# Optimization experiments

Measured on AMD Instinct MI355X. Metric: run time of the kernel, lower is better.

## Reference

```python
import jax, jax.numpy as jnp
import numpy as np

EMBED_DIM = 1024
N_HEADS = 16
HEAD_DIM = EMBED_DIM // N_HEADS


def setup_inputs() -> dict:
    key = jax.random.key(0)
    ks = jax.random.split(key, 5)
    B, T, C = 4, 2048, EMBED_DIM
    s = 0.02
    return {
        "x": jax.random.normal(ks[0], (B, T, C), dtype=jnp.float32),
        "w_qkv": jax.random.normal(ks[1], (C, 3 * C), dtype=jnp.float32) * s,
        "b_qkv": jnp.zeros((3 * C,), dtype=jnp.float32),
        "w_proj": jax.random.normal(ks[2], (C, C), dtype=jnp.float32) * s,
        "b_proj": jnp.zeros((C,), dtype=jnp.float32),
    }


def reference(x, w_qkv, b_qkv, w_proj, b_proj):
    B, T, C = x.shape
    H, D = N_HEADS, HEAD_DIM
    qkv = x @ w_qkv + b_qkv  # [B,T,3C]
    q, k, v = jnp.split(qkv, 3, axis=-1)
    # [B,H,T,D]
    q = q.reshape(B, T, H, D).transpose(0, 2, 1, 3)
    k = k.reshape(B, T, H, D).transpose(0, 2, 1, 3)
    v = v.reshape(B, T, H, D).transpose(0, 2, 1, 3)
    scale = jnp.asarray(D, x.dtype) ** -0.5
    att = jnp.einsum("bhqd,bhkd->bhqk", q, k) * scale  # [B,H,T,T]
    causal = jnp.tril(jnp.ones((T, T), dtype=bool))
    att = jnp.where(causal, att, jnp.asarray(-jnp.inf, att.dtype))
    att = jax.nn.softmax(att, axis=-1)
    out = jnp.einsum("bhqk,bhkd->bhqd", att, v)  # [B,H,T,D]
    out = out.transpose(0, 2, 1, 3).reshape(B, T, C)
    return out @ w_proj + b_proj
```

## Files before the change

kernel.cpp:

```cpp
#include <hip/hip_runtime.h>
#include <hip/hip_bf16.h>


typedef __bf16 bf16x8 __attribute__((ext_vector_type(8)));
typedef float f32x4 __attribute__((ext_vector_type(4)));
typedef unsigned short u16x8 __attribute__((ext_vector_type(8)));
typedef unsigned short u16x4 __attribute__((ext_vector_type(4)));
typedef unsigned int u32;

#define LOG2E 1.44269504088896340736f
#define NEG_INF (-__builtin_inff())

#define AS_GLOBAL(p) ((const __attribute__((address_space(1))) u32*)(p))
#define AS_LDS(p) ((__attribute__((address_space(3))) u32*)(p))

__device__ __forceinline__ unsigned short f2bf(float f) {
  unsigned int u = __builtin_bit_cast(unsigned int, f);
  u += 0x7fff + ((u >> 16) & 1);
  return (unsigned short)(u >> 16);
}

__device__ __forceinline__ u32 cvt_pk_bf16(float lo, float hi) {
  u32 r;
  asm("v_cvt_pk_bf16_f32 %0, %1, %2" : "=v"(r) : "v"(lo), "v"(hi));
  return r;
}

__device__ __forceinline__ bf16x8 ld_frag(const unsigned short* p) {
  return __builtin_bit_cast(bf16x8, *reinterpret_cast<const u16x8*>(p));
}

__global__ void k_convert(const float* __restrict__ in, unsigned short* __restrict__ out, int n4) {
  int i = blockIdx.x * blockDim.x + threadIdx.x;
  int stride = gridDim.x * blockDim.x;
  for (; i < n4; i += stride) {
    float4 v = reinterpret_cast<const float4*>(in)[i];
    u16x4 o = { f2bf(v.x), f2bf(v.y), f2bf(v.z), f2bf(v.w) };
    reinterpret_cast<u16x4*>(out)[i] = o;
  }
}

__global__ void k_transpose(const float* __restrict__ in, unsigned short* __restrict__ out,
                            int K, int N, int scaleN, float scl) {
  __shared__ float tile[32][33];
  int n0 = blockIdx.x * 32, k0 = blockIdx.y * 32;
  int tx = threadIdx.x & 31, ty = threadIdx.x >> 5;
#pragma unroll
  for (int i = 0; i < 4; i++)
    tile[ty + i * 8][tx] = in[(size_t)(k0 + ty + i * 8) * N + n0 + tx];
  __syncthreads();
#pragma unroll
  for (int i = 0; i < 4; i++) {
    int n = n0 + ty + i * 8;
    float v = tile[tx][ty + i * 8];
    if (n < scaleN) v *= scl;
    out[(size_t)n * K + k0 + tx] = f2bf(v);
  }
}

__global__ void k_scale_bias(const float* __restrict__ in, float* __restrict__ out,
                             int n, int scaleN, float scl) {
  int i = blockIdx.x * blockDim.x + threadIdx.x;
  if (i < n) out[i] = (i < scaleN) ? in[i] * scl : in[i];
}

template <bool BF16_OUT>
__global__ __launch_bounds__(256) void k_gemm(
    const unsigned short* __restrict__ A, const unsigned short* __restrict__ Bt,
    const float* __restrict__ bias, void* __restrict__ Cv, int M, int N, int K) {
  constexpr int BK = 64;
  __shared__ unsigned short Asm[128][BK];
  __shared__ unsigned short Bsm[128][BK];
  const int tid = threadIdx.x;
  const int lane = tid & 63, w = tid >> 6;
  const int wr = w >> 1, wc = w & 1;
  const int brow = blockIdx.x * 128, bcol = blockIdx.y * 128;
  const int r0 = lane & 15, kq = lane >> 4;

  f32x4 acc[4][4] = {};

  const int srow = lane >> 3;
  const int scol = ((lane & 7) ^ srow) * 8;
  const int swa = (r0 & 7) << 3;

  for (int k0 = 0; k0 < K; k0 += BK) {
    __syncthreads();
#pragma unroll
    for (int q2 = 0; q2 < 4; q2++) {
      int c = w * 4 + q2;
      const unsigned short* ga = &A[(size_t)(brow + c * 8 + srow) * K + k0 + scol];
      const unsigned short* gb = &Bt[(size_t)(bcol + c * 8 + srow) * K + k0 + scol];
      __builtin_amdgcn_global_load_lds(AS_GLOBAL(ga), AS_LDS(&Asm[c * 8][0]), 16, 0, 0);
      __builtin_amdgcn_global_load_lds(AS_GLOBAL(gb), AS_LDS(&Bsm[c * 8][0]), 16, 0, 0);
    }
    __syncthreads();
#pragma unroll
    for (int c = 0; c < 2; c++) {
      bf16x8 af[4], bfr[4];
#pragma unroll
      for (int m = 0; m < 4; m++)
        af[m] = ld_frag(&Asm[wr * 64 + m * 16 + r0][(c * 32 + kq * 8) ^ swa]);
#pragma unroll
      for (int n = 0; n < 4; n++)
        bfr[n] = ld_frag(&Bsm[wc * 64 + n * 16 + r0][(c * 32 + kq * 8) ^ swa]);
      __builtin_amdgcn_s_setprio(1);
#pragma unroll
      for (int m = 0; m < 4; m++)
#pragma unroll
        for (int n = 0; n < 4; n++)
          acc[m][n] = __builtin_amdgcn_mfma_f32_16x16x32_bf16(af[m], bfr[n], acc[m][n], 0, 0, 0);
      __builtin_amdgcn_s_setprio(0);
    }
  }

  const int orow = kq * 4;
#pragma unroll
  for (int n = 0; n < 4; n++) {
#pragma unroll
    for (int m = 0; m < 4; m++) {
      int col = bcol + wc * 64 + n * 16 + r0;
      float bv = bias[col];
#pragma unroll
      for (int r = 0; r < 4; r++) {
        int row = brow + wr * 64 + m * 16 + orow + r;
        float v = acc[m][n][r] + bv;
        if (BF16_OUT)
          ((unsigned short*)Cv)[(size_t)row * N + col] = f2bf(v);
        else
          ((float*)Cv)[(size_t)row * N + col] = v;
      }
    }
  }
}

__global__ __launch_bounds__(256, 3) void k_flash(const unsigned short* __restrict__ qkv,
                                                  unsigned short* __restrict__ att, int T) {
  constexpr int C3 = 3072, C = 1024;
  __shared__ unsigned short Ksm[2][64][72];
  __shared__ unsigned short Vsm[2][64][72];

  const int tid = threadIdx.x, lane = tid & 63, w = tid >> 6;
  const int bh = blockIdx.x;
  const int qtp = gridDim.y - 1 - blockIdx.y;
  const int b = bh >> 4, h = bh & 15;
  const int q0 = qtp * 128;
  const int r0 = lane & 15, kq = lane >> 4;

  const size_t rowbase = (size_t)b * T * C3;
  const int qb0 = q0 + w * 32, qb1 = qb0 + 16;

  bf16x8 qf[2][2];
  {
    const unsigned short* qp0 = &qkv[rowbase + (size_t)(qb0 + r0) * C3 + h * 64];
    qf[0][0] = ld_frag(&qp0[kq * 8]);
    qf[0][1] = ld_frag(&qp0[32 + kq * 8]);
    const unsigned short* qp1 = qp0 + (size_t)16 * C3;
    qf[1][0] = ld_frag(&qp1[kq * 8]);
    qf[1][1] = ld_frag(&qp1[32 + kq * 8]);
  }

  f32x4 accO[2][4] = {};
  f32x4 ls4[2] = {{0.f,0.f,0.f,0.f},{0.f,0.f,0.f,0.f}};
  float m_run[2] = {NEG_INF, NEG_INF};

  const int stk = tid >> 3, sd8 = (tid & 7) * 8;
  const unsigned short* kbase = &qkv[rowbase + (size_t)stk * C3 + h * 64 + sd8 + C];
  constexpr size_t PSTRIDE = (size_t)32 * C3;

  u16x8 kreg[2], vreg[2];
  auto LOADT = [&](size_t off) {
#pragma unroll
    for (int p = 0; p < 2; p++) {
      kreg[p] = *reinterpret_cast<const u16x8*>(kbase + off + p * PSTRIDE);
      vreg[p] = *reinterpret_cast<const u16x8*>(kbase + off + p * PSTRIDE + C);
    }
  };
  auto WRITET = [&](int buf) {
#pragma unroll
    for (int p = 0; p < 2; p++) {
      int tkk = p * 32 + stk;
      *reinterpret_cast<u16x8*>(&Ksm[buf][tkk][sd8]) = kreg[p];
      int tkx = tkk ^ sd8;
#pragma unroll
      for (int i = 0; i < 8; i++) Vsm[buf][sd8 + i][tkx] = vreg[p][i];
    }
  };

  auto TILE = [&](int buf, int k0) {
    if (k0 > qb1 + 15) return;
    const unsigned short(*Ks)[72] = Ksm[buf];
    const unsigned short(*Vs)[72] = Vsm[buf];

    f32x4 st[2][4];
    __builtin_amdgcn_s_setprio(1);
#pragma unroll
    for (int s = 0; s < 4; s++) {
      bf16x8 kf0 = ld_frag(&Ks[s * 16 + r0][kq * 8]);
      bf16x8 kf1 = ld_frag(&Ks[s * 16 + r0][32 + kq * 8]);
#pragma unroll
      for (int u = 0; u < 2; u++) {
        f32x4 a = {};
        a = __builtin_amdgcn_mfma_f32_16x16x32_bf16(kf0, qf[u][0], a, 0, 0, 0);
        a = __builtin_amdgcn_mfma_f32_16x16x32_bf16(kf1, qf[u][1], a, 0, 0, 0);
        st[u][s] = a;
      }
    }
    __builtin_amdgcn_s_setprio(0);

    u32 pd[2][2][4];
#pragma unroll
    for (int u = 0; u < 2; u++) {
      const int qbu = u ? qb1 : qb0;
      const int qmy = qbu + r0;
      f32x4 sv[4];
      if (k0 + 63 > qbu) {
#pragma unroll
        for (int s = 0; s < 4; s++)
#pragma unroll
          for (int r = 0; r < 4; r++) {
            int kg = k0 + s * 16 + kq * 4 + r;
            sv[s][r] = (kg > qmy) ? NEG_INF : st[u][s][r];
          }
      } else {
#pragma unroll
        for (int s = 0; s < 4; s++) sv[s] = st[u][s];
      }

      f32x4 m4 = __builtin_elementwise_max(__builtin_elementwise_max(sv[0], sv[1]),
                                           __builtin_elementwise_max(sv[2], sv[3]));
      float mx = fmaxf(fmaxf(m4[0], m4[1]), fmaxf(m4[2], m4[3]));

      if (__any(mx > m_run[u] + 8.f)) {
        mx = fmaxf(mx, __shfl_xor(mx, 16));
        mx = fmaxf(mx, __shfl_xor(mx, 32));
        float mn = fmaxf(m_run[u], mx);
        float corr = exp2f(m_run[u] - mn);
        m_run[u] = mn;
        ls4[u] *= corr;
        float cq[4];
#pragma unroll
        for (int r = 0; r < 4; r++) cq[r] = __shfl(corr, kq * 4 + r);
#pragma unroll
        for (int n = 0; n < 4; n++)
#pragma unroll
          for (int r = 0; r < 4; r++) accO[u][n][r] *= cq[r];
      }

#pragma unroll
      for (int s = 0; s < 4; s++) {
        f32x4 d = sv[s] - m_run[u];
        f32x4 p = { exp2f(d[0]), exp2f(d[1]), exp2f(d[2]), exp2f(d[3]) };
        sv[s] = p;
        ls4[u] += p;
      }
      pd[u][0][0] = cvt_pk_bf16(sv[0][0], sv[0][1]);
      pd[u][0][1] = cvt_pk_bf16(sv[0][2], sv[0][3]);
      pd[u][0][2] = cvt_pk_bf16(sv[1][0], sv[1][1]);
      pd[u][0][3] = cvt_pk_bf16(sv[1][2], sv[1][3]);
      pd[u][1][0] = cvt_pk_bf16(sv[2][0], sv[2][1]);
      pd[u][1][1] = cvt_pk_bf16(sv[2][2], sv[2][3]);
      pd[u][1][2] = cvt_pk_bf16(sv[3][0], sv[3][1]);
      pd[u][1][3] = cvt_pk_bf16(sv[3][2], sv[3][3]);
    }

    __builtin_amdgcn_s_setprio(1);
#pragma unroll
    for (int t = 0; t < 2; t++) {
      bf16x8 pa0 = __builtin_bit_cast(bf16x8, *reinterpret_cast<u16x8*>(pd[0][t]));
      bf16x8 pa1 = __builtin_bit_cast(bf16x8, *reinterpret_cast<u16x8*>(pd[1][t]));
#pragma unroll
      for (int n = 0; n < 4; n++) {
        int d = n * 16 + r0;
        int swzb = d & 56;
        const u16x4 lo = *reinterpret_cast<const u16x4*>(&Vs[d][(t * 32 + kq * 4) ^ swzb]);
        const u16x4 hi = *reinterpret_cast<const u16x4*>(&Vs[d][(t * 32 + 16 + kq * 4) ^ swzb]);
        u16x8 vbw;
#pragma unroll
        for (int i = 0; i < 4; i++) { vbw[i] = lo[i]; vbw[4 + i] = hi[i]; }
        bf16x8 vb = __builtin_bit_cast(bf16x8, vbw);
        accO[0][n] = __builtin_amdgcn_mfma_f32_16x16x32_bf16(pa0, vb, accO[0][n], 0, 0, 0);
        accO[1][n] = __builtin_amdgcn_mfma_f32_16x16x32_bf16(pa1, vb, accO[1][n], 0, 0, 0);
      }
    }
    __builtin_amdgcn_s_setprio(0);
  };

  int buf = 0;
  LOADT(0);
  WRITET(0);
  size_t koff = (size_t)64 * C3;
  const int nkt = (q0 + 128) >> 6;
  for (int kt = 0; kt < nkt - 1; kt++) {
    __syncthreads();
    LOADT(koff);
    koff += (size_t)64 * C3;
    TILE(buf, kt * 64);
    WRITET(buf ^ 1);
    buf ^= 1;
  }
  __syncthreads();
  TILE(buf, (nkt - 1) * 64);

#pragma unroll
  for (int u = 0; u < 2; u++) {
    const int qbu = u ? qb1 : qb0;
    float l = ls4[u][0] + ls4[u][1] + ls4[u][2] + ls4[u][3];
    l += __shfl_xor(l, 16);
    l += __shfl_xor(l, 32);
    float lr[4];
#pragma unroll
    for (int r = 0; r < 4; r++) lr[r] = 1.f / __shfl(l, kq * 4 + r);
#pragma unroll
    for (int n = 0; n < 4; n++) {
#pragma unroll
      for (int r = 0; r < 4; r++) {
        int qrow = qbu + kq * 4 + r;
        float v = accO[u][n][r] * lr[r];
        att[((size_t)b * T + qrow) * C + h * 64 + n * 16 + r0] = f2bf(v);
      }
    }
  }
}

extern "C" void kernel_launch(void* const* d_in, const int* in_sizes, int n_in,
                              void* d_out, int out_size, void* d_ws, size_t ws_size,
                              hipStream_t stream) {
  const float* x = (const float*)d_in[0];
  const float* w_qkv = (const float*)d_in[1];
  const float* b_qkv = (const float*)d_in[2];
  const float* w_proj = (const float*)d_in[3];
  const float* b_proj = (const float*)d_in[4];

  constexpr int B = 4, T = 2048, C = 1024, C3 = 3072;
  constexpr int M = B * T;
  constexpr float SCL = 0.125f * LOG2E;

  unsigned short* x_bf = (unsigned short*)d_ws;
  unsigned short* wqkvT = x_bf + (size_t)M * C;
  unsigned short* wprojT = wqkvT + (size_t)C3 * C;
  unsigned short* qkv = wprojT + (size_t)C * C;
  unsigned short* att = qkv + (size_t)M * C3;
  float* bias_s = (float*)(att + (size_t)M * C);

  hipLaunchKernelGGL(k_convert, dim3(2048), dim3(256), 0, stream, x, x_bf, M * C / 4);
  hipLaunchKernelGGL(k_transpose, dim3(C3 / 32, C / 32), dim3(256), 0, stream,
                     w_qkv, wqkvT, C, C3, C, SCL);
  hipLaunchKernelGGL(k_transpose, dim3(C / 32, C / 32), dim3(256), 0, stream,
                     w_proj, wprojT, C, C, 0, 1.f);
  hipLaunchKernelGGL(k_scale_bias, dim3((C3 + 255) / 256), dim3(256), 0, stream,
                     b_qkv, bias_s, C3, C, SCL);
  hipLaunchKernelGGL((k_gemm<true>), dim3(M / 128, C3 / 128), dim3(256), 0, stream,
                     x_bf, wqkvT, bias_s, (void*)qkv, M, C3, C);
  hipLaunchKernelGGL(k_flash, dim3(64, 16), dim3(256), 0, stream, qkv, att, T);
  hipLaunchKernelGGL((k_gemm<false>), dim3(M / 128, C / 128), dim3(256), 0, stream,
                     att, wprojT, b_proj, d_out, M, C, C);
}
```

Before: 166.9 us.

## Double flash-attention query tile to 256 rows per block for K/V reuse

Each flash-attention block now covers 256 query rows instead of 128, so each wave handles 64 rows across four 16-row sub-tiles. K/V tiles staged in LDS are reused across twice as many queries, which halves global K/V traffic and the number of blocks. Causal skipping is applied per pair of sub-tiles. The cost is higher register pressure, with launch bounds lowered to 2 blocks per CU, and only 512 blocks in the grid, which risks worse load balance across the causal triangle.

```diff
diff --git a/kernel.cpp b/kernel.cpp
--- a/kernel.cpp
+++ b/kernel.cpp
@@ -133,7 +133,7 @@
   }
 }
 
-__global__ __launch_bounds__(256, 3) void k_flash(const unsigned short* __restrict__ qkv,
+__global__ __launch_bounds__(256, 2) void k_flash(const unsigned short* __restrict__ qkv,
                                                   unsigned short* __restrict__ att, int T) {
   constexpr int C3 = 3072, C = 1024;
   __shared__ unsigned short Ksm[2][64][72];
@@ -143,25 +143,23 @@
   const int bh = blockIdx.x;
   const int qtp = gridDim.y - 1 - blockIdx.y;
   const int b = bh >> 4, h = bh & 15;
-  const int q0 = qtp * 128;
+  const int q0 = qtp * 256;
   const int r0 = lane & 15, kq = lane >> 4;
 
   const size_t rowbase = (size_t)b * T * C3;
-  const int qb0 = q0 + w * 32, qb1 = qb0 + 16;
-
-  bf16x8 qf[2][2];
-  {
-    const unsigned short* qp0 = &qkv[rowbase + (size_t)(qb0 + r0) * C3 + h * 64];
-    qf[0][0] = ld_frag(&qp0[kq * 8]);
-    qf[0][1] = ld_frag(&qp0[32 + kq * 8]);
-    const unsigned short* qp1 = qp0 + (size_t)16 * C3;
-    qf[1][0] = ld_frag(&qp1[kq * 8]);
-    qf[1][1] = ld_frag(&qp1[32 + kq * 8]);
-  }
-
-  f32x4 accO[2][4] = {};
-  f32x4 ls4[2] = {{0.f,0.f,0.f,0.f},{0.f,0.f,0.f,0.f}};
-  float m_run[2] = {NEG_INF, NEG_INF};
+  const int qb0 = q0 + w * 64;
+
+  bf16x8 qf[4][2];
+#pragma unroll
+  for (int u = 0; u < 4; u++) {
+    const unsigned short* qp = &qkv[rowbase + (size_t)(qb0 + u * 16 + r0) * C3 + h * 64];
+    qf[u][0] = ld_frag(&qp[kq * 8]);
+    qf[u][1] = ld_frag(&qp[32 + kq * 8]);
+  }
+
+  f32x4 accO[4][4] = {};
+  f32x4 ls4[4] = {{0.f,0.f,0.f,0.f},{0.f,0.f,0.f,0.f},{0.f,0.f,0.f,0.f},{0.f,0.f,0.f,0.f}};
+  float m_run[4] = {NEG_INF, NEG_INF, NEG_INF, NEG_INF};
 
   const int stk = tid >> 3, sd8 = (tid & 7) * 8;
   const unsigned short* kbase = &qkv[rowbase + (size_t)stk * C3 + h * 64 + sd8 + C];
@@ -187,87 +185,95 @@
   };
 
   auto TILE = [&](int buf, int k0) {
-    if (k0 > qb1 + 15) return;
+    if (k0 > qb0 + 63) return;
+    const bool p0 = (k0 <= qb0 + 31);
     const unsigned short(*Ks)[72] = Ksm[buf];
     const unsigned short(*Vs)[72] = Vsm[buf];
 
-    f32x4 st[2][4];
+    u32 pd[4][2][4];
+
+#pragma unroll
+    for (int pp = 0; pp < 2; pp++) {
+      if (pp == 0 && !p0) continue;
+      f32x4 st[2][4];
+      __builtin_amdgcn_s_setprio(1);
+#pragma unroll
+      for (int s = 0; s < 4; s++) {
+        bf16x8 kf0 = ld_frag(&Ks[s * 16 + r0][kq * 8]);
+        bf16x8 kf1 = ld_frag(&Ks[s * 16 + r0][32 + kq * 8]);
+#pragma unroll
+        for (int ui = 0; ui < 2; ui++) {
+          const int u = pp * 2 + ui;
+          f32x4 a = {};
+          a = __builtin_amdgcn_mfma_f32_16x16x32_bf16(kf0, qf[u][0], a, 0, 0, 0);
+          a = __builtin_amdgcn_mfma_f32_16x16x32_bf16(kf1, qf[u][1], a, 0, 0, 0);
+          st[ui][s] = a;
+        }
+      }
+      __builtin_amdgcn_s_setprio(0);
+
+#pragma unroll
+      for (int ui = 0; ui < 2; ui++) {
+        const int u = pp * 2 + ui;
+        const int qbu = qb0 + u * 16;
+        const int qmy = qbu + r0;
+        f32x4 sv[4];
+        if (k0 + 63 > qbu) {
+#pragma unroll
+          for (int s = 0; s < 4; s++)
+#pragma unroll
+            for (int r = 0; r < 4; r++) {
+              int kg = k0 + s * 16 + kq * 4 + r;
+              sv[s][r] = (kg > qmy) ? NEG_INF : st[ui][s][r];
+            }
+        } else {
+#pragma unroll
+          for (int s = 0; s < 4; s++) sv[s] = st[ui][s];
+        }
+
+        f32x4 m4 = __builtin_elementwise_max(__builtin_elementwise_max(sv[0], sv[1]),
+                                             __builtin_elementwise_max(sv[2], sv[3]));
+        float mx = fmaxf(fmaxf(m4[0], m4[1]), fmaxf(m4[2], m4[3]));
+
+        if (__any(mx > m_run[u] + 8.f)) {
+          mx = fmaxf(mx, __shfl_xor(mx, 16));
+          mx = fmaxf(mx, __shfl_xor(mx, 32));
+          float mn = fmaxf(m_run[u], mx);
+          float corr = exp2f(m_run[u] - mn);
+          m_run[u] = mn;
+          ls4[u] *= corr;
+          float cq[4];
+#pragma unroll
+          for (int r = 0; r < 4; r++) cq[r] = __shfl(corr, kq * 4 + r);
+#pragma unroll
+          for (int n = 0; n < 4; n++)
+#pragma unroll
+            for (int r = 0; r < 4; r++) accO[u][n][r] *= cq[r];
+        }
+
+#pragma unroll
+        for (int s = 0; s < 4; s++) {
+          f32x4 d = sv[s] - m_run[u];
+          f32x4 p = { exp2f(d[0]), exp2f(d[1]), exp2f(d[2]), exp2f(d[3]) };
+          sv[s] = p;
+          ls4[u] += p;
+        }
+        pd[u][0][0] = cvt_pk_bf16(sv[0][0], sv[0][1]);
+        pd[u][0][1] = cvt_pk_bf16(sv[0][2], sv[0][3]);
+        pd[u][0][2] = cvt_pk_bf16(sv[1][0], sv[1][1]);
+        pd[u][0][3] = cvt_pk_bf16(sv[1][2], sv[1][3]);
+        pd[u][1][0] = cvt_pk_bf16(sv[2][0], sv[2][1]);
+        pd[u][1][1] = cvt_pk_bf16(sv[2][2], sv[2][3]);
+        pd[u][1][2] = cvt_pk_bf16(sv[3][0], sv[3][1]);
+        pd[u][1][3] = cvt_pk_bf16(sv[3][2], sv[3][3]);
+      }
+    }
+
     __builtin_amdgcn_s_setprio(1);
 #pragma unroll
-    for (int s = 0; s < 4; s++) {
-      bf16x8 kf0 = ld_frag(&Ks[s * 16 + r0][kq * 8]);
-      bf16x8 kf1 = ld_frag(&Ks[s * 16 + r0][32 + kq * 8]);
-#pragma unroll
-      for (int u = 0; u < 2; u++) {
-        f32x4 a = {};
-        a = __builtin_amdgcn_mfma_f32_16x16x32_bf16(kf0, qf[u][0], a, 0, 0, 0);
-        a = __builtin_amdgcn_mfma_f32_16x16x32_bf16(kf1, qf[u][1], a, 0, 0, 0);
-        st[u][s] = a;
-      }
-    }
-    __builtin_amdgcn_s_setprio(0);
-
-    u32 pd[2][2][4];
-#pragma unroll
-    for (int u = 0; u < 2; u++) {
-      const int qbu = u ? qb1 : qb0;
-      const int qmy = qbu + r0;
-      f32x4 sv[4];
-      if (k0 + 63 > qbu) {
-#pragma unroll
-        for (int s = 0; s < 4; s++)
-#pragma unroll
-          for (int r = 0; r < 4; r++) {
-            int kg = k0 + s * 16 + kq * 4 + r;
-            sv[s][r] = (kg > qmy) ? NEG_INF : st[u][s][r];
-          }
-      } else {
-#pragma unroll
-        for (int s = 0; s < 4; s++) sv[s] = st[u][s];
-      }
-
-      f32x4 m4 = __builtin_elementwise_max(__builtin_elementwise_max(sv[0], sv[1]),
-                                           __builtin_elementwise_max(sv[2], sv[3]));
-      float mx = fmaxf(fmaxf(m4[0], m4[1]), fmaxf(m4[2], m4[3]));
-
-      if (__any(mx > m_run[u] + 8.f)) {
-        mx = fmaxf(mx, __shfl_xor(mx, 16));
-        mx = fmaxf(mx, __shfl_xor(mx, 32));
-        float mn = fmaxf(m_run[u], mx);
-        float corr = exp2f(m_run[u] - mn);
-        m_run[u] = mn;
-        ls4[u] *= corr;
-        float cq[4];
-#pragma unroll
-        for (int r = 0; r < 4; r++) cq[r] = __shfl(corr, kq * 4 + r);
-#pragma unroll
-        for (int n = 0; n < 4; n++)
-#pragma unroll
-          for (int r = 0; r < 4; r++) accO[u][n][r] *= cq[r];
-      }
-
-#pragma unroll
-      for (int s = 0; s < 4; s++) {
-        f32x4 d = sv[s] - m_run[u];
-        f32x4 p = { exp2f(d[0]), exp2f(d[1]), exp2f(d[2]), exp2f(d[3]) };
-        sv[s] = p;
-        ls4[u] += p;
-      }
-      pd[u][0][0] = cvt_pk_bf16(sv[0][0], sv[0][1]);
-      pd[u][0][1] = cvt_pk_bf16(sv[0][2], sv[0][3]);
-      pd[u][0][2] = cvt_pk_bf16(sv[1][0], sv[1][1]);
-      pd[u][0][3] = cvt_pk_bf16(sv[1][2], sv[1][3]);
-      pd[u][1][0] = cvt_pk_bf16(sv[2][0], sv[2][1]);
-      pd[u][1][1] = cvt_pk_bf16(sv[2][2], sv[2][3]);
-      pd[u][1][2] = cvt_pk_bf16(sv[3][0], sv[3][1]);
-      pd[u][1][3] = cvt_pk_bf16(sv[3][2], sv[3][3]);
-    }
-
-    __builtin_amdgcn_s_setprio(1);
-#pragma unroll
     for (int t = 0; t < 2; t++) {
-      bf16x8 pa0 = __builtin_bit_cast(bf16x8, *reinterpret_cast<u16x8*>(pd[0][t]));
-      bf16x8 pa1 = __builtin_bit_cast(bf16x8, *reinterpret_cast<u16x8*>(pd[1][t]));
+      bf16x8 pa2 = __builtin_bit_cast(bf16x8, *reinterpret_cast<u16x8*>(pd[2][t]));
+      bf16x8 pa3 = __builtin_bit_cast(bf16x8, *reinterpret_cast<u16x8*>(pd[3][t]));
 #pragma unroll
       for (int n = 0; n < 4; n++) {
         int d = n * 16 + r0;
@@ -278,8 +284,14 @@
 #pragma unroll
         for (int i = 0; i < 4; i++) { vbw[i] = lo[i]; vbw[4 + i] = hi[i]; }
         bf16x8 vb = __builtin_bit_cast(bf16x8, vbw);
-        accO[0][n] = __builtin_amdgcn_mfma_f32_16x16x32_bf16(pa0, vb, accO[0][n], 0, 0, 0);
-        accO[1][n] = __builtin_amdgcn_mfma_f32_16x16x32_bf16(pa1, vb, accO[1][n], 0, 0, 0);
+        accO[2][n] = __builtin_amdgcn_mfma_f32_16x16x32_bf16(pa2, vb, accO[2][n], 0, 0, 0);
+        accO[3][n] = __builtin_amdgcn_mfma_f32_16x16x32_bf16(pa3, vb, accO[3][n], 0, 0, 0);
+        if (p0) {
+          bf16x8 pa0 = __builtin_bit_cast(bf16x8, *reinterpret_cast<u16x8*>(pd[0][t]));
+          bf16x8 pa1 = __builtin_bit_cast(bf16x8, *reinterpret_cast<u16x8*>(pd[1][t]));
+          accO[0][n] = __builtin_amdgcn_mfma_f32_16x16x32_bf16(pa0, vb, accO[0][n], 0, 0, 0);
+          accO[1][n] = __builtin_amdgcn_mfma_f32_16x16x32_bf16(pa1, vb, accO[1][n], 0, 0, 0);
+        }
       }
     }
     __builtin_amdgcn_s_setprio(0);
@@ -289,7 +301,7 @@
   LOADT(0);
   WRITET(0);
   size_t koff = (size_t)64 * C3;
-  const int nkt = (q0 + 128) >> 6;
+  const int nkt = (q0 + 256) >> 6;
   for (int kt = 0; kt < nkt - 1; kt++) {
     __syncthreads();
     LOADT(koff);
@@ -302,8 +314,8 @@
   TILE(buf, (nkt - 1) * 64);
 
 #pragma unroll
-  for (int u = 0; u < 2; u++) {
-    const int qbu = u ? qb1 : qb0;
+  for (int u = 0; u < 4; u++) {
+    const int qbu = qb0 + u * 16;
     float l = ls4[u][0] + ls4[u][1] + ls4[u][2] + ls4[u][3];
     l += __shfl_xor(l, 16);
     l += __shfl_xor(l, 32);
@@ -351,7 +363,7 @@
                      b_qkv, bias_s, C3, C, SCL);
   hipLaunchKernelGGL((k_gemm<true>), dim3(M / 128, C3 / 128), dim3(256), 0, stream,
                      x_bf, wqkvT, bias_s, (void*)qkv, M, C3, C);
-  hipLaunchKernelGGL(k_flash, dim3(64, 16), dim3(256), 0, stream, qkv, att, T);
+  hipLaunchKernelGGL(k_flash, dim3(64, 8), dim3(256), 0, stream, qkv, att, T);
   hipLaunchKernelGGL((k_gemm<false>), dim3(M / 128, C / 128), dim3(256), 0, stream,
                      att, wprojT, b_proj, d_out, M, C, C);
 }
```

Result: slower. 190.1 us (+13.9%).
